# Optimization experiments

Hardware: AMD Instinct MI355X
Metric: run time of the kernel (lower is better)

The kernel has to match this reference:

```python
import jax, jax.numpy as jnp
import numpy as np

B, S, H = 4, 2048, 576
NH, NKV, HD = 9, 3, 64  # num heads, kv heads, head_dim
ROPE_THETA = 100000.0
NEG = -1e9


def _rope_cos_sin(seq_len, dim, base, dtype):
    inv_freq = 1.0 / (base ** (jnp.arange(0, dim, 2, dtype=jnp.float32) / dim))
    t = jnp.arange(seq_len, dtype=jnp.float32)
    freqs = jnp.outer(t, inv_freq)            # [S, dim/2]
    emb = jnp.concatenate([freqs, freqs], -1)  # [S, dim]
    return jnp.cos(emb).astype(dtype), jnp.sin(emb).astype(dtype)


def _rotate_half(x):
    x1, x2 = x[..., : x.shape[-1] // 2], x[..., x.shape[-1] // 2 :]
    return jnp.concatenate([-x2, x1], axis=-1)


def setup_inputs() -> dict:
    key = jax.random.key(0)
    kx, kq, kk, kv, ko = jax.random.split(key, 5)
    x = jax.random.normal(kx, (B, S, H), dtype=jnp.float32)
    sc = 1.0 / np.sqrt(H)
    Wq = jax.random.normal(kq, (NH * HD, H), dtype=jnp.float32) * sc
    Wk = jax.random.normal(kk, (NKV * HD, H), dtype=jnp.float32) * sc
    Wv = jax.random.normal(kv, (NKV * HD, H), dtype=jnp.float32) * sc
    Wo = jax.random.normal(ko, (H, NH * HD), dtype=jnp.float32) * sc
    # additive causal mask [1,1,S,S]
    causal = jnp.tril(jnp.ones((S, S), dtype=bool))
    mask = jnp.where(causal, 0.0, NEG).astype(jnp.float32)[None, None]
    return {"x": x, "Wq": Wq, "Wk": Wk, "Wv": Wv, "Wo": Wo, "mask": mask}


def reference(x, Wq, Wk, Wv, Wo, mask):
    b, s, _ = x.shape
    q = (x @ Wq.T).reshape(b, s, NH, HD).transpose(0, 2, 1, 3)    # [b,nh,s,hd]
    k = (x @ Wk.T).reshape(b, s, NKV, HD).transpose(0, 2, 1, 3)   # [b,nkv,s,hd]
    v = (x @ Wv.T).reshape(b, s, NKV, HD).transpose(0, 2, 1, 3)
    cos, sin = _rope_cos_sin(s, HD, ROPE_THETA, x.dtype)          # [s,hd]
    cos, sin = cos[None, None], sin[None, None]
    q = q * cos + _rotate_half(q) * sin
    k = k * cos + _rotate_half(k) * sin
    groups = NH // NKV
    k = jnp.repeat(k, groups, axis=1)                              # [b,nh,s,hd]
    v = jnp.repeat(v, groups, axis=1)
    scores = jnp.einsum("bhqd,bhkd->bhqk", q, k) / np.sqrt(HD)
    scores = scores + mask
    attn = jax.nn.softmax(scores.astype(jnp.float32), axis=-1).astype(q.dtype)
    out = jnp.einsum("bhqk,bhkd->bhqd", attn, v)                   # [b,nh,s,hd]
    out = out.transpose(0, 2, 1, 3).reshape(b, s, NH * HD)
    return out @ Wo.T
```

## Files before the change

### kernel.cpp

```cpp
#include <hip/hip_runtime.h>
#include <hip/hip_bf16.h>
#include <cstdint>

typedef float  fvec4  __attribute__((ext_vector_type(4)));
typedef float  f32x4  __attribute__((ext_vector_type(4)));
typedef float  f32x16 __attribute__((ext_vector_type(16)));
typedef short  bvec8  __attribute__((ext_vector_type(8)));
typedef short  bvec4  __attribute__((ext_vector_type(4)));
typedef unsigned int uint;

#define B_    4
#define S_    2048
#define H_    576
#define NH_   9
#define NKV_  3
#define HD_   64
#define M_    8192
#define KVD_  192

static __device__ __forceinline__ short f2bf(float f) {
  __hip_bfloat16 h = __float2bfloat16(f);
  short s;
  __builtin_memcpy(&s, &h, 2);
  return s;
}

static __device__ __forceinline__ float fexp2(float x) {
  float r;
  asm("v_exp_f32 %0, %1" : "=v"(r) : "v"(x));
  return r;
}

static __device__ __forceinline__ uint cvtpk(float lo, float hi) {
  uint r;
  asm("v_cvt_pk_bf16_f32 %0, %1, %2" : "=v"(r) : "v"(lo), "v"(hi));
  return r;
}

static __device__ __forceinline__ void plswap(uint& a, uint& b) {
  asm volatile("v_permlane32_swap_b32 %0, %1" : "+v"(a), "+v"(b));
}

static __device__ __forceinline__ void gload16(void* lds, const void* g) {
  __builtin_amdgcn_global_load_lds((const __attribute__((address_space(1))) void*)g,
                                   (__attribute__((address_space(3))) void*)lds, 16, 0, 0);
}

__global__ __launch_bounds__(256) void rope_table_kernel(float* __restrict__ ct,
                                                         float* __restrict__ st) {
  int idx = blockIdx.x * 256 + threadIdx.x;
  int s = idx >> 5, i = idx & 31;
  float invf = powf(100000.0f, -(float)i / 32.0f);
  float fr = (float)s * invf;
  float sv, cv;
  sincosf(fr, &sv, &cv);
  ct[idx] = cv;
  st[idx] = sv;
}

__global__ __launch_bounds__(256) void convert_x_kernel(const float* __restrict__ in,
                                                        short* __restrict__ out, int n4) {
  int i = blockIdx.x * 256 + threadIdx.x;
  if (i >= n4) return;
  fvec4 v = *(const fvec4*)(in + (long)i * 4);
  bvec4 o;
  o[0] = f2bf(v[0]); o[1] = f2bf(v[1]); o[2] = f2bf(v[2]); o[3] = f2bf(v[3]);
  *(bvec4*)(out + (long)i * 4) = o;
}

__global__ __launch_bounds__(256) void convert_w_kernel(const float* __restrict__ wq,
                                                        const float* __restrict__ wk,
                                                        const float* __restrict__ wv,
                                                        const float* __restrict__ wo,
                                                        short* __restrict__ out) {
  long e = ((long)blockIdx.x * 256 + threadIdx.x) * 4;
  const float* src; long off;
  if (e < 331776)        { src = wq; off = e; }
  else if (e < 442368)   { src = wk; off = e - 331776; }
  else if (e < 552960)   { src = wv; off = e - 442368; }
  else                   { src = wo; off = e - 552960; }
  fvec4 v = *(const fvec4*)(src + off);
  bvec4 o;
  o[0] = f2bf(v[0]); o[1] = f2bf(v[1]); o[2] = f2bf(v[2]); o[3] = f2bf(v[3]);
  *(bvec4*)(out + e) = o;
}

__global__ __launch_bounds__(256) void qkv_gemm_fused(const short* __restrict__ A,
                                                      const short* __restrict__ W,
                                                      const float* __restrict__ ct,
                                                      const float* __restrict__ st,
                                                      short* __restrict__ qb,
                                                      short* __restrict__ kb,
                                                      short* __restrict__ vt) {
  __shared__ __align__(16) char lds_raw[49152];
  short* As = (short*)lds_raw;
  short* Ws = (short*)(lds_raw + 32768);
  const int K = H_;
  const int t = threadIdx.x;
  const int lane = t & 63;
  const int w = t >> 6;
  const int wm = w >> 1, wn = w & 1;
  const long m0 = (long)blockIdx.x * 128;
  const int by = blockIdx.y;
  const long n0 = (long)by * 64;
  const int lc = lane & 15, lg = lane >> 4;
  const int nk = K >> 6;

  const int r0 = t >> 3, c0 = t & 7;
  const short* asrc = A + (m0 + r0) * (long)K + ((c0 ^ (r0 & 7)) << 3);
  const short* wsrc = W + (n0 + r0) * (long)K + ((c0 ^ (r0 & 7)) << 3);
  const int dba = (t & 192) * 8;

  f32x4 acc[4][2];
#pragma unroll
  for (int i = 0; i < 4; ++i)
#pragma unroll
    for (int j = 0; j < 2; ++j) acc[i][j] = (f32x4){0.f, 0.f, 0.f, 0.f};

#define QKV_STAGE(buf)                                                         \
  do {                                                                         \
    short* asd = As + (buf) * 8192;                                            \
    short* wsd = Ws + (buf) * 4096;                                            \
    _Pragma("unroll")                                                          \
    for (int it = 0; it < 4; ++it)                                             \
      gload16(asd + dba + it * 2048, asrc + (long)32 * it * K);                \
    _Pragma("unroll")                                                          \
    for (int it = 0; it < 2; ++it)                                             \
      gload16(wsd + dba + it * 2048, wsrc + (long)32 * it * K);                \
    asrc += 64; wsrc += 64;                                                    \
  } while (0)

  QKV_STAGE(0);

  for (int ks = 0; ks < nk; ++ks) {
    const int cur = ks & 1;
    __builtin_amdgcn_s_barrier();
    if (ks + 1 < nk) {
      QKV_STAGE(1 - cur);
      asm volatile("s_waitcnt vmcnt(6)" ::: "memory");
    } else {
      asm volatile("s_waitcnt vmcnt(0)" ::: "memory");
    }
    __builtin_amdgcn_s_barrier();
    const short* as_ = As + cur * 8192;
    const short* ws_ = Ws + cur * 4096;
#pragma unroll
    for (int kk = 0; kk < 2; ++kk) {
      bvec8 af[4], bfr[2];
#pragma unroll
      for (int mt = 0; mt < 4; ++mt) {
        int r = wm * 64 + mt * 16 + lc;
        af[mt] = *(const bvec8*)(as_ + r * 64 + (((kk * 4 + lg) ^ (r & 7)) << 3));
      }
#pragma unroll
      for (int nt = 0; nt < 2; ++nt) {
        int r = wn * 32 + nt * 16 + lc;
        bfr[nt] = *(const bvec8*)(ws_ + r * 64 + (((kk * 4 + lg) ^ (r & 7)) << 3));
      }
#pragma unroll
      for (int mt = 0; mt < 4; ++mt)
#pragma unroll
        for (int nt = 0; nt < 2; ++nt)
          acc[mt][nt] = __builtin_amdgcn_mfma_f32_16x16x32_bf16(af[mt], bfr[nt],
                                                                acc[mt][nt], 0, 0, 0);
    }
  }
#undef QKV_STAGE

  __syncthreads();
  float* tile = (float*)lds_raw;
#pragma unroll
  for (int mt = 0; mt < 4; ++mt)
#pragma unroll
    for (int nt = 0; nt < 2; ++nt)
#pragma unroll
      for (int r = 0; r < 4; ++r)
        tile[(wm * 64 + mt * 16 + lg * 4 + r) * 65 + wn * 32 + nt * 16 + lc] = acc[mt][nt][r];
  __syncthreads();

  if (by < 12) {
    const float scale = (by < 9) ? 0.18033688011112042f : 1.0f;
    const int r = t >> 1, i0 = (t & 1) * 16;
    const long srow = m0 + r;
    const int spos = (int)(srow & (S_ - 1));
    float lo[16], hi[16];
#pragma unroll
    for (int jj = 0; jj < 4; ++jj) {
      fvec4 cv = *(const fvec4*)(ct + spos * 32 + i0 + jj * 4);
      fvec4 sv = *(const fvec4*)(st + spos * 32 + i0 + jj * 4);
#pragma unroll
      for (int k = 0; k < 4; ++k) {
        int j = jj * 4 + k;
        float a = tile[r * 65 + i0 + j];
        float b = tile[r * 65 + i0 + j + 32];
        lo[j] = (a * cv[k] - b * sv[k]) * scale;
        hi[j] = (b * cv[k] + a * sv[k]) * scale;
      }
    }
    uint pl[4], ph[4];
#pragma unroll
    for (int g = 0; g < 4; ++g) {
      pl[g] = cvtpk(lo[2 * g], lo[2 * g + 1]);
      ph[g] = cvtpk(hi[2 * g], hi[2 * g + 1]);
    }
    uint pl2[4], ph2[4];
#pragma unroll
    for (int g = 0; g < 4; ++g) {
      pl2[g] = cvtpk(lo[8 + 2 * g], lo[9 + 2 * g]);
      ph2[g] = cvtpk(hi[8 + 2 * g], hi[9 + 2 * g]);
    }
    short* dst = (by < 9) ? (qb + srow * H_ + (long)by * 64 + i0)
                          : (kb + srow * KVD_ + (long)(by - 9) * 64 + i0);
    uint4 s0; s0.x = pl[0];  s0.y = pl[1];  s0.z = pl[2];  s0.w = pl[3];
    uint4 s1; s1.x = pl2[0]; s1.y = pl2[1]; s1.z = pl2[2]; s1.w = pl2[3];
    uint4 s2; s2.x = ph[0];  s2.y = ph[1];  s2.z = ph[2];  s2.w = ph[3];
    uint4 s3; s3.x = ph2[0]; s3.y = ph2[1]; s3.z = ph2[2]; s3.w = ph2[3];
    *(uint4*)(dst)          = s0;
    *(uint4*)(dst + 8)      = s1;
    *(uint4*)(dst + 32)     = s2;
    *(uint4*)(dst + 40)     = s3;
  } else {
    const int d = t & 63, sc0 = (t >> 6) * 32;
    const int kvh = by - 12;
    const int b = (int)(m0 >> 11);
    float v[32];
#pragma unroll
    for (int j = 0; j < 32; ++j) v[j] = tile[(sc0 + j) * 65 + d];
    uint pk_[16];
#pragma unroll
    for (int g = 0; g < 16; ++g) pk_[g] = cvtpk(v[2 * g], v[2 * g + 1]);
    short* dst = vt + ((long)((b * NKV_ + kvh) * HD_ + d)) * S_ + (m0 & (S_ - 1)) + sc0;
#pragma unroll
    for (int q4 = 0; q4 < 4; ++q4) {
      uint4 sv_; sv_.x = pk_[4 * q4]; sv_.y = pk_[4 * q4 + 1];
      sv_.z = pk_[4 * q4 + 2]; sv_.w = pk_[4 * q4 + 3];
      *(uint4*)(dst + q4 * 8) = sv_;
    }
  }
}

#define GEMM_STAGE(buf)                                                        \
  do {                                                                         \
    short* asd = As + (buf) * 8192;                                            \
    short* wsd = Ws + (buf) * 4096;                                            \
    _Pragma("unroll")                                                          \
    for (int it = 0; it < 4; ++it)                                             \
      gload16(asd + dba + it * 2048, asrc + (long)32 * it * K);                \
    _Pragma("unroll")                                                          \
    for (int it = 0; it < 2; ++it)                                             \
      gload16(wsd + dba + it * 2048, wsrc + (long)32 * it * K);                \
    asrc += 64; wsrc += 64;                                                    \
  } while (0)

__global__ __launch_bounds__(256) void gemm_mfma_kernel(const short* __restrict__ A,
                                                        const short* __restrict__ W,
                                                        float* __restrict__ C,
                                                        int M, int N, int K) {
  __shared__ __align__(16) short As[2 * 128 * 64];
  __shared__ __align__(16) short Ws[2 * 64 * 64];
  const int t = threadIdx.x;
  const int lane = t & 63;
  const int w = t >> 6;
  const int wm = w >> 1, wn = w & 1;
  const long m0 = (long)blockIdx.x * 128;
  const long n0 = (long)blockIdx.y * 64;
  const int lc = lane & 15, lg = lane >> 4;
  const int nk = K >> 6;

  const int r0 = t >> 3, c0 = t & 7;
  const short* asrc = A + (m0 + r0) * (long)K + ((c0 ^ (r0 & 7)) << 3);
  const short* wsrc = W + (n0 + r0) * (long)K + ((c0 ^ (r0 & 7)) << 3);
  const int dba = (t & 192) * 8;

  f32x4 acc[4][2];
#pragma unroll
  for (int i = 0; i < 4; ++i)
#pragma unroll
    for (int j = 0; j < 2; ++j) acc[i][j] = (f32x4){0.f, 0.f, 0.f, 0.f};

  GEMM_STAGE(0);

  for (int ks = 0; ks < nk; ++ks) {
    const int cur = ks & 1;
    __builtin_amdgcn_s_barrier();
    if (ks + 1 < nk) {
      GEMM_STAGE(1 - cur);
      asm volatile("s_waitcnt vmcnt(6)" ::: "memory");
    } else {
      asm volatile("s_waitcnt vmcnt(0)" ::: "memory");
    }
    __builtin_amdgcn_s_barrier();
    const short* as_ = As + cur * 8192;
    const short* ws_ = Ws + cur * 4096;
#pragma unroll
    for (int kk = 0; kk < 2; ++kk) {
      bvec8 af[4], bfr[2];
#pragma unroll
      for (int mt = 0; mt < 4; ++mt) {
        int r = wm * 64 + mt * 16 + lc;
        af[mt] = *(const bvec8*)(as_ + r * 64 + (((kk * 4 + lg) ^ (r & 7)) << 3));
      }
#pragma unroll
      for (int nt = 0; nt < 2; ++nt) {
        int r = wn * 32 + nt * 16 + lc;
        bfr[nt] = *(const bvec8*)(ws_ + r * 64 + (((kk * 4 + lg) ^ (r & 7)) << 3));
      }
#pragma unroll
      for (int mt = 0; mt < 4; ++mt)
#pragma unroll
        for (int nt = 0; nt < 2; ++nt)
          acc[mt][nt] = __builtin_amdgcn_mfma_f32_16x16x32_bf16(af[mt], bfr[nt],
                                                                acc[mt][nt], 0, 0, 0);
    }
  }

#pragma unroll
  for (int mt = 0; mt < 4; ++mt)
#pragma unroll
    for (int nt = 0; nt < 2; ++nt)
#pragma unroll
      for (int r = 0; r < 4; ++r) {
        long row = m0 + wm * 64 + mt * 16 + lg * 4 + r;
        long col = n0 + wn * 32 + nt * 16 + lc;
        C[row * (long)N + col] = acc[mt][nt][r];
      }
}

#define ATTN_STAGE(buf)                                                        \
  do {                                                                         \
    short* kd = Ks + (buf) * 4096;                                             \
    short* vd = Vs + (buf) * 4096;                                             \
    _Pragma("unroll")                                                          \
    for (int it = 0; it < 4; ++it) {                                           \
      gload16(kd + dbw + it * 1024, ksrc + (long)16 * it * KVD_);              \
      gload16(vd + dbw + it * 1024, vsrc + (long)16 * it * S_);                \
    }                                                                          \
    ksrc += 64 * KVD_;  vsrc += 64;                                            \
  } while (0)

__global__ __launch_bounds__(128) void attn2w_kernel(const short* __restrict__ qb,
                                                     const short* __restrict__ kb,
                                                     const short* __restrict__ vt,
                                                     short* __restrict__ ao) {
  __shared__ __align__(16) short Ks[2 * 64 * 64];
  __shared__ __align__(16) short Vs[2 * 64 * 64];
  const int t  = threadIdx.x;
  const int w  = t >> 6;
  const int l  = t & 63;
  const int lq = l & 31;
  const int h2 = l >> 5;
  const int qt = 31 - (int)blockIdx.x;
  const int hq = blockIdx.y, b = blockIdx.z;
  const int kvh = hq / 3;
  const int q0 = qt * 64;
  const int q  = q0 + w * 32 + lq;
  const int nkv = qt + 1;
  const int bS = b * S_;

  const int r0 = t >> 3, c0 = t & 7;
  const int sw0 = (c0 ^ (r0 & 7)) << 3;
  const short* ksrc = kb + ((long)(bS + r0)) * KVD_ + kvh * HD_ + sw0;
  const short* vsrc = vt + ((long)((b * NKV_ + kvh) * HD_ + r0)) * S_ + sw0;
  const int dbw = (t & 64) * 8;

  bvec8 qfr[4];
  {
    const short* qp = qb + ((long)(bS + q)) * H_ + hq * HD_ + h2 * 8;
#pragma unroll
    for (int c = 0; c < 4; ++c) qfr[c] = *(const bvec8*)(qp + c * 16);
  }

  f32x16 ot[2];
#pragma unroll
  for (int r = 0; r < 16; ++r) { ot[0][r] = 0.f; ot[1][r] = 0.f; }
  float l_run = 0.f;

  ATTN_STAGE(0);

  for (int kv = 0; kv < nkv; ++kv) {
    const int cur = kv & 1;
    __builtin_amdgcn_s_barrier();
    if (kv + 1 < nkv) {
      ATTN_STAGE(1 - cur);
      asm volatile("s_waitcnt vmcnt(8)" ::: "memory");
    } else {
      asm volatile("s_waitcnt vmcnt(0)" ::: "memory");
    }
    __builtin_amdgcn_s_barrier();

    const short* ks_ = Ks + cur * 4096;
    const short* vs_ = Vs + cur * 4096;

    f32x16 sc[2];
#pragma unroll
    for (int r = 0; r < 16; ++r) { sc[0][r] = 0.f; sc[1][r] = 0.f; }
    __builtin_amdgcn_s_setprio(1);
#pragma unroll
    for (int s = 0; s < 2; ++s) {
      int r = s * 32 + lq;
#pragma unroll
      for (int c = 0; c < 4; ++c) {
        bvec8 kf = *(const bvec8*)(ks_ + r * 64 + (((2 * c + h2) ^ (r & 7)) << 3));
        sc[s] = __builtin_amdgcn_mfma_f32_32x32x16_bf16(kf, qfr[c], sc[s], 0, 0, 0);
      }
    }
    __builtin_amdgcn_s_setprio(0);

    if (kv == nkv - 1) {
#pragma unroll
      for (int s = 0; s < 2; ++s)
#pragma unroll
        for (int r = 0; r < 16; ++r) {
          int key = q0 + s * 32 + (r & 3) + ((r >> 2) << 3) + h2 * 4;
          if (key > q) sc[s][r] = -1e30f;
        }
    }

#pragma unroll
    for (int s = 0; s < 2; ++s)
#pragma unroll
      for (int r = 0; r < 16; ++r) sc[s][r] = fexp2(sc[s][r]);

    float red[16];
#pragma unroll
    for (int i = 0; i < 16; ++i) red[i] = sc[0][i] + sc[1][i];
#pragma unroll
    for (int off = 8; off >= 1; off >>= 1)
#pragma unroll
      for (int i = 0; i < off; ++i) red[i] += red[i + off];
    l_run += red[0] + __shfl_xor(red[0], 32);

    uint pa[2][4], pb[2][4];
#pragma unroll
    for (int s = 0; s < 2; ++s)
#pragma unroll
      for (int g = 0; g < 4; ++g) {
        pa[s][g] = cvtpk(sc[s][4 * g],     sc[s][4 * g + 1]);
        pb[s][g] = cvtpk(sc[s][4 * g + 2], sc[s][4 * g + 3]);
      }
    bvec8 pfr[4];
#pragma unroll
    for (int kc = 0; kc < 4; ++kc) {
      const int s = kc >> 1, m = kc & 1;
      uint x0 = pa[s][2 * m], x1 = pa[s][2 * m + 1];
      uint y0 = pb[s][2 * m], y1 = pb[s][2 * m + 1];
      plswap(x0, x1);
      plswap(y0, y1);
      union { uint u[4]; bvec8 v; } c_;
      c_.u[0] = x0; c_.u[1] = y0; c_.u[2] = x1; c_.u[3] = y1;
      pfr[kc] = c_.v;
    }

    __builtin_amdgcn_s_setprio(1);
#pragma unroll
    for (int dt = 0; dt < 2; ++dt) {
      int rv = dt * 32 + lq;
#pragma unroll
      for (int kc = 0; kc < 4; ++kc) {
        bvec8 vf_ = *(const bvec8*)(vs_ + rv * 64 + (((2 * kc + h2) ^ (rv & 7)) << 3));
        ot[dt] = __builtin_amdgcn_mfma_f32_32x32x16_bf16(vf_, pfr[kc], ot[dt], 0, 0, 0);
      }
    }
    __builtin_amdgcn_s_setprio(0);
  }

  const float inv = 1.0f / l_run;
  const long orow = (long)(bS + q);
#pragma unroll
  for (int dt = 0; dt < 2; ++dt)
#pragma unroll
    for (int g = 0; g < 4; ++g) {
      uint w0 = cvtpk(ot[dt][4 * g] * inv,     ot[dt][4 * g + 1] * inv);
      uint w1 = cvtpk(ot[dt][4 * g + 2] * inv, ot[dt][4 * g + 3] * inv);
      int d = dt * 32 + 8 * g + 4 * h2;
      uint2 stv; stv.x = w0; stv.y = w1;
      *(uint2*)(ao + orow * H_ + hq * HD_ + d) = stv;
    }
}

extern "C" void kernel_launch(void* const* d_in, const int* in_sizes, int n_in,
                              void* d_out, int out_size, void* d_ws, size_t ws_size,
                              hipStream_t stream) {
  const float* x  = (const float*)d_in[0];
  const float* Wq = (const float*)d_in[1];
  const float* Wk = (const float*)d_in[2];
  const float* Wv = (const float*)d_in[3];
  const float* Wo = (const float*)d_in[4];
  float* out = (float*)d_out;

  char* p = (char*)d_ws;
  float* ct  = (float*)p;  p += (long)S_ * 32 * 4;
  float* st  = (float*)p;  p += (long)S_ * 32 * 4;
  short* xb  = (short*)p;  p += (long)M_ * H_ * 2;
  short* w16 = (short*)p;  p += 884736L * 2;
  short* qb  = (short*)p;  p += (long)M_ * H_ * 2;
  short* kb  = (short*)p;  p += (long)M_ * KVD_ * 2;
  short* vt  = (short*)p;  p += (long)M_ * KVD_ * 2;
  short* ao  = (short*)p;  p += (long)M_ * H_ * 2;
  short* wo16 = w16 + 552960;

  rope_table_kernel<<<256, 256, 0, stream>>>(ct, st);
  convert_x_kernel<<<(M_ * H_ / 4 + 255) / 256, 256, 0, stream>>>(x, xb, M_ * H_ / 4);
  convert_w_kernel<<<864, 256, 0, stream>>>(Wq, Wk, Wv, Wo, w16);

  qkv_gemm_fused<<<dim3(64, 15), 256, 0, stream>>>(xb, w16, ct, st, qb, kb, vt);

  attn2w_kernel<<<dim3(32, NH_, B_), 128, 0, stream>>>(qb, kb, vt, ao);

  gemm_mfma_kernel<<<dim3(64, 9), 256, 0, stream>>>(ao, wo16, out, M_, H_, H_);
}
```

Baseline: 202.0 us.

## Pair causal query tiles per block and remap blocks for balanced KV-group scheduling

Each attention block now handles two query tiles, pair and 31-pair, so every block processes a constant 33 KV tiles in total and causal work is load-balanced. Both tiles share each staged K/V tile in shared memory, which halves the K/V loads for the shorter tile. Blocks are remapped on a 1D grid so that the work of one batch and KV-head group is spread across what appear to be 8 XCD-strided slots, likely to improve L2 reuse. The cost is extra registers for the second Q fragment and accumulator set, which may lower occupancy.

```diff
diff --git a/kernel.cpp b/kernel.cpp
--- a/kernel.cpp
+++ b/kernel.cpp
@@ -326,6 +326,94 @@
       }
 }
 
+static __device__ __forceinline__ void qk_mfma(f32x16 sc[2], const bvec8 qfr[4],
+                                               const short* ks_, int lq, int h2) {
+#pragma unroll
+  for (int r = 0; r < 16; ++r) { sc[0][r] = 0.f; sc[1][r] = 0.f; }
+#pragma unroll
+  for (int s = 0; s < 2; ++s) {
+    int r = s * 32 + lq;
+#pragma unroll
+    for (int c = 0; c < 4; ++c) {
+      bvec8 kf = *(const bvec8*)(ks_ + r * 64 + (((2 * c + h2) ^ (r & 7)) << 3));
+      sc[s] = __builtin_amdgcn_mfma_f32_32x32x16_bf16(kf, qfr[c], sc[s], 0, 0, 0);
+    }
+  }
+}
+
+static __device__ __forceinline__ void mask_tile(f32x16 sc[2], int kb0, int q, int h2) {
+#pragma unroll
+  for (int s = 0; s < 2; ++s)
+#pragma unroll
+    for (int r = 0; r < 16; ++r) {
+      int key = kb0 + s * 32 + (r & 3) + ((r >> 2) << 3) + h2 * 4;
+      if (key > q) sc[s][r] = -1e30f;
+    }
+}
+
+static __device__ __forceinline__ void softmax_pv(f32x16 sc[2], f32x16 ot[2],
+                                                  float& l_run, const short* vs_,
+                                                  int lq, int h2) {
+#pragma unroll
+  for (int s = 0; s < 2; ++s)
+#pragma unroll
+    for (int r = 0; r < 16; ++r) sc[s][r] = fexp2(sc[s][r]);
+  float red[16];
+#pragma unroll
+  for (int i = 0; i < 16; ++i) red[i] = sc[0][i] + sc[1][i];
+#pragma unroll
+  for (int off = 8; off >= 1; off >>= 1)
+#pragma unroll
+    for (int i = 0; i < off; ++i) red[i] += red[i + off];
+  l_run += red[0] + __shfl_xor(red[0], 32);
+  uint pa[2][4], pb[2][4];
+#pragma unroll
+  for (int s = 0; s < 2; ++s)
+#pragma unroll
+    for (int g = 0; g < 4; ++g) {
+      pa[s][g] = cvtpk(sc[s][4 * g],     sc[s][4 * g + 1]);
+      pb[s][g] = cvtpk(sc[s][4 * g + 2], sc[s][4 * g + 3]);
+    }
+  bvec8 pfr[4];
+#pragma unroll
+  for (int kc = 0; kc < 4; ++kc) {
+    const int s = kc >> 1, m = kc & 1;
+    uint x0 = pa[s][2 * m], x1 = pa[s][2 * m + 1];
+    uint y0 = pb[s][2 * m], y1 = pb[s][2 * m + 1];
+    plswap(x0, x1);
+    plswap(y0, y1);
+    union { uint u[4]; bvec8 v; } c_;
+    c_.u[0] = x0; c_.u[1] = y0; c_.u[2] = x1; c_.u[3] = y1;
+    pfr[kc] = c_.v;
+  }
+  __builtin_amdgcn_s_setprio(1);
+#pragma unroll
+  for (int dt = 0; dt < 2; ++dt) {
+    int rv = dt * 32 + lq;
+#pragma unroll
+    for (int kc = 0; kc < 4; ++kc) {
+      bvec8 vf_ = *(const bvec8*)(vs_ + rv * 64 + (((2 * kc + h2) ^ (rv & 7)) << 3));
+      ot[dt] = __builtin_amdgcn_mfma_f32_32x32x16_bf16(vf_, pfr[kc], ot[dt], 0, 0, 0);
+    }
+  }
+  __builtin_amdgcn_s_setprio(0);
+}
+
+static __device__ __forceinline__ void attn_epilogue(const f32x16 ot[2], float l_run,
+                                                     short* ao, long orow, int hq, int h2) {
+  const float inv = 1.0f / l_run;
+#pragma unroll
+  for (int dt = 0; dt < 2; ++dt)
+#pragma unroll
+    for (int g = 0; g < 4; ++g) {
+      uint w0 = cvtpk(ot[dt][4 * g] * inv,     ot[dt][4 * g + 1] * inv);
+      uint w1 = cvtpk(ot[dt][4 * g + 2] * inv, ot[dt][4 * g + 3] * inv);
+      int d = dt * 32 + 8 * g + 4 * h2;
+      uint2 stv; stv.x = w0; stv.y = w1;
+      *(uint2*)(ao + orow * H_ + hq * HD_ + d) = stv;
+    }
+}
+
 #define ATTN_STAGE(buf)                                                        \
   do {                                                                         \
     short* kd = Ks + (buf) * 4096;                                             \
@@ -338,10 +426,10 @@
     ksrc += 64 * KVD_;  vsrc += 64;                                            \
   } while (0)
 
-__global__ __launch_bounds__(128) void attn2w_kernel(const short* __restrict__ qb,
-                                                     const short* __restrict__ kb,
-                                                     const short* __restrict__ vt,
-                                                     short* __restrict__ ao) {
+__global__ __launch_bounds__(128) void attn_pair_kernel(const short* __restrict__ qb,
+                                                        const short* __restrict__ kb,
+                                                        const short* __restrict__ vt,
+                                                        short* __restrict__ ao) {
   __shared__ __align__(16) short Ks[2 * 64 * 64];
   __shared__ __align__(16) short Vs[2 * 64 * 64];
   const int t  = threadIdx.x;
@@ -349,13 +437,23 @@
   const int l  = t & 63;
   const int lq = l & 31;
   const int h2 = l >> 5;
-  const int qt = 31 - (int)blockIdx.x;
-  const int hq = blockIdx.y, b = blockIdx.z;
-  const int kvh = hq / 3;
-  const int q0 = qt * 64;
-  const int q  = q0 + w * 32 + lq;
-  const int nkv = qt + 1;
-  const int bS = b * S_;
+
+  const int bid = (int)blockIdx.x;
+  const int g   = bid & 7;
+  const int wkr = 72 * g + (bid >> 3);
+  const int combo = wkr / 48;
+  const int jj  = wkr - combo * 48;
+  const int b   = combo / 3;
+  const int kvh = combo - b * 3;
+  const int hq  = kvh * 3 + (jj >> 4);
+  const int pair = jj & 15;
+
+  const int qA0 = pair * 64;
+  const int qB0 = (31 - pair) * 64;
+  const int nkv = 32 - pair;
+  const int bS  = b * S_;
+  const int qA  = qA0 + w * 32 + lq;
+  const int qB  = qB0 + w * 32 + lq;
 
   const int r0 = t >> 3, c0 = t & 7;
   const int sw0 = (c0 ^ (r0 & 7)) << 3;
@@ -363,22 +461,30 @@
   const short* vsrc = vt + ((long)((b * NKV_ + kvh) * HD_ + r0)) * S_ + sw0;
   const int dbw = (t & 64) * 8;
 
-  bvec8 qfr[4];
+  bvec8 qfrA[4], qfrB[4];
   {
-    const short* qp = qb + ((long)(bS + q)) * H_ + hq * HD_ + h2 * 8;
-#pragma unroll
-    for (int c = 0; c < 4; ++c) qfr[c] = *(const bvec8*)(qp + c * 16);
-  }
-
-  f32x16 ot[2];
-#pragma unroll
-  for (int r = 0; r < 16; ++r) { ot[0][r] = 0.f; ot[1][r] = 0.f; }
-  float l_run = 0.f;
+    const short* qpa = qb + ((long)(bS + qA)) * H_ + hq * HD_ + h2 * 8;
+    const short* qpb = qb + ((long)(bS + qB)) * H_ + hq * HD_ + h2 * 8;
+#pragma unroll
+    for (int c = 0; c < 4; ++c) {
+      qfrA[c] = *(const bvec8*)(qpa + c * 16);
+      qfrB[c] = *(const bvec8*)(qpb + c * 16);
+    }
+  }
+
+  f32x16 otA[2], otB[2];
+#pragma unroll
+  for (int r = 0; r < 16; ++r) {
+    otA[0][r] = 0.f; otA[1][r] = 0.f;
+    otB[0][r] = 0.f; otB[1][r] = 0.f;
+  }
+  float lA = 0.f, lB = 0.f;
 
   ATTN_STAGE(0);
 
   for (int kv = 0; kv < nkv; ++kv) {
     const int cur = kv & 1;
+    const int kb0 = kv * 64;
     __builtin_amdgcn_s_barrier();
     if (kv + 1 < nkv) {
       ATTN_STAGE(1 - cur);
@@ -390,92 +496,22 @@
 
     const short* ks_ = Ks + cur * 4096;
     const short* vs_ = Vs + cur * 4096;
-
-    f32x16 sc[2];
-#pragma unroll
-    for (int r = 0; r < 16; ++r) { sc[0][r] = 0.f; sc[1][r] = 0.f; }
-    __builtin_amdgcn_s_setprio(1);
-#pragma unroll
-    for (int s = 0; s < 2; ++s) {
-      int r = s * 32 + lq;
-#pragma unroll
-      for (int c = 0; c < 4; ++c) {
-        bvec8 kf = *(const bvec8*)(ks_ + r * 64 + (((2 * c + h2) ^ (r & 7)) << 3));
-        sc[s] = __builtin_amdgcn_mfma_f32_32x32x16_bf16(kf, qfr[c], sc[s], 0, 0, 0);
-      }
-    }
-    __builtin_amdgcn_s_setprio(0);
-
-    if (kv == nkv - 1) {
-#pragma unroll
-      for (int s = 0; s < 2; ++s)
-#pragma unroll
-        for (int r = 0; r < 16; ++r) {
-          int key = q0 + s * 32 + (r & 3) + ((r >> 2) << 3) + h2 * 4;
-          if (key > q) sc[s][r] = -1e30f;
-        }
-    }
-
-#pragma unroll
-    for (int s = 0; s < 2; ++s)
-#pragma unroll
-      for (int r = 0; r < 16; ++r) sc[s][r] = fexp2(sc[s][r]);
-
-    float red[16];
-#pragma unroll
-    for (int i = 0; i < 16; ++i) red[i] = sc[0][i] + sc[1][i];
-#pragma unroll
-    for (int off = 8; off >= 1; off >>= 1)
-#pragma unroll
-      for (int i = 0; i < off; ++i) red[i] += red[i + off];
-    l_run += red[0] + __shfl_xor(red[0], 32);
-
-    uint pa[2][4], pb[2][4];
-#pragma unroll
-    for (int s = 0; s < 2; ++s)
-#pragma unroll
-      for (int g = 0; g < 4; ++g) {
-        pa[s][g] = cvtpk(sc[s][4 * g],     sc[s][4 * g + 1]);
-        pb[s][g] = cvtpk(sc[s][4 * g + 2], sc[s][4 * g + 3]);
-      }
-    bvec8 pfr[4];
-#pragma unroll
-    for (int kc = 0; kc < 4; ++kc) {
-      const int s = kc >> 1, m = kc & 1;
-      uint x0 = pa[s][2 * m], x1 = pa[s][2 * m + 1];
-      uint y0 = pb[s][2 * m], y1 = pb[s][2 * m + 1];
-      plswap(x0, x1);
-      plswap(y0, y1);
-      union { uint u[4]; bvec8 v; } c_;
-      c_.u[0] = x0; c_.u[1] = y0; c_.u[2] = x1; c_.u[3] = y1;
-      pfr[kc] = c_.v;
-    }
-
-    __builtin_amdgcn_s_setprio(1);
-#pragma unroll
-    for (int dt = 0; dt < 2; ++dt) {
-      int rv = dt * 32 + lq;
-#pragma unroll
-      for (int kc = 0; kc < 4; ++kc) {
-        bvec8 vf_ = *(const bvec8*)(vs_ + rv * 64 + (((2 * kc + h2) ^ (rv & 7)) << 3));
-        ot[dt] = __builtin_amdgcn_mfma_f32_32x32x16_bf16(vf_, pfr[kc], ot[dt], 0, 0, 0);
-      }
-    }
-    __builtin_amdgcn_s_setprio(0);
-  }
-
-  const float inv = 1.0f / l_run;
-  const long orow = (long)(bS + q);
-#pragma unroll
-  for (int dt = 0; dt < 2; ++dt)
-#pragma unroll
-    for (int g = 0; g < 4; ++g) {
-      uint w0 = cvtpk(ot[dt][4 * g] * inv,     ot[dt][4 * g + 1] * inv);
-      uint w1 = cvtpk(ot[dt][4 * g + 2] * inv, ot[dt][4 * g + 3] * inv);
-      int d = dt * 32 + 8 * g + 4 * h2;
-      uint2 stv; stv.x = w0; stv.y = w1;
-      *(uint2*)(ao + orow * H_ + hq * HD_ + d) = stv;
-    }
+    const bool doA = (kv <= pair);
+
+    f32x16 scB[2];
+    qk_mfma(scB, qfrB, ks_, lq, h2);
+    f32x16 scA[2];
+    if (doA) qk_mfma(scA, qfrA, ks_, lq, h2);
+
+    if (kv == nkv - 1) mask_tile(scB, kb0, qB, h2);
+    if (doA && kv == pair) mask_tile(scA, kb0, qA, h2);
+
+    softmax_pv(scB, otB, lB, vs_, lq, h2);
+    if (doA) softmax_pv(scA, otA, lA, vs_, lq, h2);
+  }
+
+  attn_epilogue(otA, lA, ao, (long)(bS + qA), hq, h2);
+  attn_epilogue(otB, lB, ao, (long)(bS + qB), hq, h2);
 }
 
 extern "C" void kernel_launch(void* const* d_in, const int* in_sizes, int n_in,
@@ -505,7 +541,7 @@
 
   qkv_gemm_fused<<<dim3(64, 15), 256, 0, stream>>>(xb, w16, ct, st, qb, kb, vt);
 
-  attn2w_kernel<<<dim3(32, NH_, B_), 128, 0, stream>>>(qb, kb, vt, ao);
+  attn_pair_kernel<<<576, 128, 0, stream>>>(qb, kb, vt, ao);
 
   gemm_mfma_kernel<<<dim3(64, 9), 256, 0, stream>>>(ao, wo16, out, M_, H_, H_);
 }
```

Measured after the change: 193.3 us. -4.3%, faster.
